# Performance work log

Hardware: AMD Instinct MI355X
Metric: run time of the kernel (lower is better)

The kernel has to match this reference:

```python
import jax, jax.numpy as jnp
import numpy as np

N, E = 50000, 800000
IN_CH, OUT_CH = 128, 16
H1, D1 = 2, 2 * OUT_CH           # conv1: heads=2, per-head dim 32, concat -> 64
MID = H1 * D1                    # 64
NEG_SLOPE = 0.2

def setup_inputs() -> dict:
    key = jax.random.key(0)
    ks = jax.random.split(key, 16)
    s = lambda k, shape: jax.random.normal(k, shape, dtype=jnp.float32) * 0.1
    return {
        "x": jax.random.normal(ks[0], (N, IN_CH), dtype=jnp.float32),
        "edge_index": jax.random.randint(ks[1], (2, E), 0, N, dtype=jnp.int64),
        "W1": s(ks[2], (IN_CH, H1 * D1)),
        "att_src1": s(ks[3], (H1, D1)),
        "att_dst1": s(ks[4], (H1, D1)),
        "b1": jnp.zeros((MID,), jnp.float32),
        "W_mu": s(ks[5], (MID, OUT_CH)),
        "att_src_mu": s(ks[6], (1, OUT_CH)),
        "att_dst_mu": s(ks[7], (1, OUT_CH)),
        "b_mu": jnp.zeros((OUT_CH,), jnp.float32),
        "W_ls": s(ks[8], (MID, OUT_CH)),
        "att_src_ls": s(ks[9], (1, OUT_CH)),
        "att_dst_ls": s(ks[10], (1, OUT_CH)),
        "b_ls": jnp.zeros((OUT_CH,), jnp.float32),
    }

def gat_conv(x, src, dst, W, att_src, att_dst, bias, heads, d):
    # x: [N, F]; src/dst: [E'] (self loops included); PyG GATConv, eval mode (dropout off)
    n = x.shape[0]
    h = (x @ W).reshape(n, heads, d)                     # [N, H, D]
    a_src = jnp.sum(h * att_src, axis=-1)                # [N, H]
    a_dst = jnp.sum(h * att_dst, axis=-1)                # [N, H]
    e = jax.nn.leaky_relu(a_src[src] + a_dst[dst], NEG_SLOPE)   # [E', H]
    # segment softmax over incoming edges of each destination node
    m = jax.ops.segment_max(e, dst, num_segments=n)
    ex = jnp.exp(e - m[dst])
    denom = jax.ops.segment_sum(ex, dst, num_segments=n)
    alpha = ex / (denom[dst] + 1e-16)                    # [E', H]
    msg = h[src] * alpha[:, :, None]                     # [E', H, D]
    out = jax.ops.segment_sum(msg, dst, num_segments=n)  # [N, H, D]
    return out, bias

def reference(x, edge_index, W1, att_src1, att_dst1, b1,
              W_mu, att_src_mu, att_dst_mu, b_mu,
              W_ls, att_src_ls, att_dst_ls, b_ls):
    n = x.shape[0]
    loops = jnp.arange(n, dtype=edge_index.dtype)
    src = jnp.concatenate([edge_index[0], loops])        # add_self_loops=True (inputs have none)
    dst = jnp.concatenate([edge_index[1], loops])
    h, b = gat_conv(x, src, dst, W1, att_src1, att_dst1, b1, H1, D1)
    h = jax.nn.relu(h.reshape(n, H1 * D1) + b)           # concat=True -> [N, 64]
    mu, bm = gat_conv(h, src, dst, W_mu, att_src_mu, att_dst_mu, b_mu, 1, OUT_CH)
    ls, bl = gat_conv(h, src, dst, W_ls, att_src_ls, att_dst_ls, b_ls, 1, OUT_CH)
    mu = mu.mean(axis=1) + bm                            # concat=False, heads=1 -> mean == squeeze
    ls = ls.mean(axis=1) + bl
    return (mu, ls)
```

## Files before the change

### kernel.cpp

```cpp
#include <hip/hip_runtime.h>

#define NEG 0.2f

__device__ __forceinline__ float lrelu(float v) { return v > 0.f ? v : NEG * v; }

__device__ __forceinline__ unsigned short f2bf(float f) {
    unsigned u = __float_as_uint(f);
    unsigned r = (u + 0x7FFF + ((u >> 16) & 1)) >> 16;
    return (unsigned short)r;
}
__device__ __forceinline__ float bf_lo(unsigned v) { return __uint_as_float(v << 16); }
__device__ __forceinline__ float bf_hi(unsigned v) { return __uint_as_float(v & 0xffff0000u); }

__global__ void build_w1ext(const float* __restrict__ W1, const float* __restrict__ asrc,
                            const float* __restrict__ adst, float* __restrict__ Wext) {
    int i = blockIdx.x * blockDim.x + threadIdx.x;
    if (i >= 128 * 68) return;
    int k = i / 68, c = i % 68;
    if (c < 64) { Wext[i] = W1[k * 64 + c]; return; }
    int j = c - 64;
    int hh = j & 1;
    const float* att = (j >= 2) ? adst : asrc;
    float s = 0.f;
    for (int d = 0; d < 32; ++d) s += W1[k * 64 + hh * 32 + d] * att[hh * 32 + d];
    Wext[i] = s;
}

__global__ void build_w2ext(const float* __restrict__ Wmu, const float* __restrict__ Wls,
                            const float* __restrict__ asmu, const float* __restrict__ admu,
                            const float* __restrict__ asls, const float* __restrict__ adls,
                            float* __restrict__ Wext) {
    int i = blockIdx.x * blockDim.x + threadIdx.x;
    if (i >= 64 * 36) return;
    int k = i / 36, c = i % 36;
    if (c < 16) { Wext[i] = Wmu[k * 16 + c]; return; }
    if (c < 32) { Wext[i] = Wls[k * 16 + (c - 16)]; return; }
    int j = c - 32;
    const float* W = (j < 2) ? Wmu : Wls;
    const float* att = (j == 0) ? asmu : (j == 1) ? admu : (j == 2) ? asls : adls;
    float s = 0.f;
    for (int c2 = 0; c2 < 16; ++c2) s += W[k * 16 + c2] * att[c2];
    Wext[i] = s;
}

__global__ __launch_bounds__(256) void gemm1(const float* __restrict__ x,
                                             const float* __restrict__ Wext,
                                             unsigned* __restrict__ h32, float* __restrict__ a1, int n) {
    __shared__ float xs[16][129];
    __shared__ float Ws[128][68];
    int t = threadIdx.x;
    int row0 = blockIdx.x * 16;
    for (int i = t; i < 128 * 68; i += 256) Ws[i / 68][i % 68] = Wext[i];
    for (int i = t; i < 16 * 128; i += 256) {
        int r = i >> 7, k = i & 127;
        int gr = row0 + r;
        xs[r][k] = (gr < n) ? x[gr * 128 + k] : 0.f;
    }
    __syncthreads();
    int r = t >> 4, c = t & 15;
    float acc0 = 0, acc1 = 0, acc2 = 0, acc3 = 0;
    for (int k = 0; k < 128; ++k) {
        float xv = xs[r][k];
        acc0 += xv * Ws[k][c * 4 + 0];
        acc1 += xv * Ws[k][c * 4 + 1];
        acc2 += xv * Ws[k][c * 4 + 2];
        acc3 += xv * Ws[k][c * 4 + 3];
    }
    int gr = row0 + r;
    if (gr < n) {
        unsigned p0 = ((unsigned)f2bf(acc1) << 16) | f2bf(acc0);
        unsigned p1 = ((unsigned)f2bf(acc3) << 16) | f2bf(acc2);
        *(uint2*)&h32[gr * 32 + c * 2] = make_uint2(p0, p1);
    }
    if (t < 64) {
        int r2 = t >> 2, j = t & 3;
        float a = 0.f;
        for (int k = 0; k < 128; ++k) a += xs[r2][k] * Ws[k][64 + j];
        if (row0 + r2 < n) a1[(row0 + r2) * 4 + j] = a;
    }
}

__global__ void count_deg(const int* __restrict__ dstv, int E, int* __restrict__ deg) {
    int i = blockIdx.x * blockDim.x + threadIdx.x;
    if (i < E) atomicAdd(&deg[dstv[i]], 1);
}

__global__ __launch_bounds__(256) void block_sums(const int* __restrict__ deg, int n,
                                                  int* __restrict__ bsums) {
    int i = blockIdx.x * 256 + threadIdx.x;
    int v = (i < n) ? deg[i] : 0;
    for (int o = 32; o > 0; o >>= 1) v += __shfl_down(v, o, 64);
    __shared__ int ws[4];
    if ((threadIdx.x & 63) == 0) ws[threadIdx.x >> 6] = v;
    __syncthreads();
    if (threadIdx.x == 0) bsums[blockIdx.x] = ws[0] + ws[1] + ws[2] + ws[3];
}

__global__ __launch_bounds__(256) void scan_bsums(int* __restrict__ bsums, int nb) {
    __shared__ int s[256];
    int t = threadIdx.x;
    int v = (t < nb) ? bsums[t] : 0;
    s[t] = v;
    __syncthreads();
    for (int o = 1; o < 256; o <<= 1) {
        int u = (t >= o) ? s[t - o] : 0;
        __syncthreads();
        s[t] += u;
        __syncthreads();
    }
    if (t < nb) bsums[t] = s[t] - v;
}

__global__ __launch_bounds__(256) void write_offs(const int* __restrict__ deg,
                                                  const int* __restrict__ bsums, int n,
                                                  int* __restrict__ offs, int* __restrict__ cursor) {
    int t = threadIdx.x;
    int i = blockIdx.x * 256 + t;
    int v = (i < n) ? deg[i] : 0;
    __shared__ int s[256];
    s[t] = v;
    __syncthreads();
    for (int o = 1; o < 256; o <<= 1) {
        int u = (t >= o) ? s[t - o] : 0;
        __syncthreads();
        s[t] += u;
        __syncthreads();
    }
    int excl = s[t] - v + bsums[blockIdx.x];
    if (i < n) { offs[i] = excl; cursor[i] = excl; }
    if (i == n - 1) offs[n] = excl + v;
}

__global__ void scatter_edges(const int* __restrict__ srcv, const int* __restrict__ dstv, int E,
                              int* __restrict__ cursor, int* __restrict__ srcs) {
    int i = blockIdx.x * blockDim.x + threadIdx.x;
    if (i < E) {
        int d = dstv[i];
        int slot = atomicAdd(&cursor[d], 1);
        srcs[slot] = srcv[i];
    }
}

__global__ __launch_bounds__(256) void agg1(const unsigned* __restrict__ h32, const float* __restrict__ a1,
                                            const int* __restrict__ offs, const int* __restrict__ srcs,
                                            const float* __restrict__ b1, float* __restrict__ h1, int n) {
    int wid = threadIdx.x >> 6, lane = threadIdx.x & 63;
    int node = blockIdx.x * 4 + wid;
    if (node >= n) return;
    int half = lane >> 5;
    int l = lane & 31;
    int head = l >> 4;
    float adst = a1[node * 4 + 2 + head];
    float acc0 = 0.f, acc1 = 0.f, denom = 0.f;
    if (half == 0) {
        float w = __expf(lrelu(a1[node * 4 + head] + adst));
        unsigned hv = h32[node * 32 + l];
        acc0 = w * bf_lo(hv); acc1 = w * bf_hi(hv);
        denom = w;
    }
    int kb = offs[node], ke = offs[node + 1];
    for (int k = kb + half; k < ke; k += 2) {
        int s = srcs[k];
        float wv = __expf(lrelu(a1[s * 4 + head] + adst));
        unsigned hv = h32[s * 32 + l];
        denom += wv;
        acc0 += wv * bf_lo(hv);
        acc1 += wv * bf_hi(hv);
    }
    acc0  += __shfl(acc0,  lane ^ 32, 64);
    acc1  += __shfl(acc1,  lane ^ 32, 64);
    denom += __shfl(denom, lane ^ 32, 64);
    if (half == 0) {
        float o0 = acc0 / denom + b1[2 * l];
        float o1 = acc1 / denom + b1[2 * l + 1];
        *(float2*)&h1[node * 64 + 2 * l] = make_float2(fmaxf(o0, 0.f), fmaxf(o1, 0.f));
    }
}

__global__ __launch_bounds__(256) void gemm2(const float* __restrict__ h1,
                                             const float* __restrict__ Wext,
                                             unsigned* __restrict__ hml, float* __restrict__ a2, int n) {
    __shared__ float hs[16][65];
    __shared__ float Ws[64][36];
    int t = threadIdx.x;
    int row0 = blockIdx.x * 16;
    for (int i = t; i < 64 * 36; i += 256) Ws[i / 36][i % 36] = Wext[i];
    for (int i = t; i < 16 * 64; i += 256) {
        int r = i >> 6, k = i & 63;
        int gr = row0 + r;
        hs[r][k] = (gr < n) ? h1[gr * 64 + k] : 0.f;
    }
    __syncthreads();
    int r = t >> 4, c = t & 15;
    float am = 0, al = 0;
    for (int k = 0; k < 64; ++k) {
        float hv = hs[r][k];
        am += hv * Ws[k][c];
        al += hv * Ws[k][16 + c];
    }
    int gr = row0 + r;
    if (gr < n) hml[gr * 16 + c] = ((unsigned)f2bf(al) << 16) | f2bf(am);
    if (t < 64) {
        int r2 = t >> 2, j = t & 3;
        float a = 0.f;
        for (int k = 0; k < 64; ++k) a += hs[r2][k] * Ws[k][32 + j];
        if (row0 + r2 < n) a2[(row0 + r2) * 4 + j] = a;
    }
}

__global__ __launch_bounds__(256) void agg2(const unsigned* __restrict__ hml,
                                            const float* __restrict__ a2, const int* __restrict__ offs,
                                            const int* __restrict__ srcs,
                                            const float* __restrict__ bmu, const float* __restrict__ bls,
                                            float* __restrict__ out, int n) {
    int grp = threadIdx.x >> 5;
    int node = blockIdx.x * 8 + grp;
    if (node >= n) return;
    int lane32 = threadIdx.x & 31;
    int half = lane32 >> 4;
    int c = lane32 & 15;
    float admu = a2[node * 4 + 1], adls = a2[node * 4 + 3];
    float amu = 0.f, als = 0.f, dmu = 0.f, dls = 0.f;
    if (half == 0) {
        float wmu = __expf(lrelu(a2[node * 4 + 0] + admu));
        float wls = __expf(lrelu(a2[node * 4 + 2] + adls));
        unsigned hv = hml[node * 16 + c];
        amu = wmu * bf_lo(hv); als = wls * bf_hi(hv);
        dmu = wmu; dls = wls;
    }
    int kb = offs[node], ke = offs[node + 1];
    for (int k = kb + half; k < ke; k += 2) {
        int s = srcs[k];
        float4 av = *(const float4*)&a2[s * 4];
        float w1v = __expf(lrelu(av.x + admu));
        float w2v = __expf(lrelu(av.z + adls));
        unsigned hv = hml[s * 16 + c];
        dmu += w1v; dls += w2v;
        amu += w1v * bf_lo(hv);
        als += w2v * bf_hi(hv);
    }
    amu += __shfl_xor(amu, 16, 64);
    als += __shfl_xor(als, 16, 64);
    dmu += __shfl_xor(dmu, 16, 64);
    dls += __shfl_xor(dls, 16, 64);
    if (half == 0) {
        out[node * 16 + c] = amu / dmu + bmu[c];
        out[(size_t)n * 16 + node * 16 + c] = als / dls + bls[c];
    }
}

extern "C" void kernel_launch(void* const* d_in, const int* in_sizes, int n_in,
                              void* d_out, int out_size, void* d_ws, size_t ws_size,
                              hipStream_t stream) {
    const float* x    = (const float*)d_in[0];
    const int*   ei   = (const int*)d_in[1];
    const float* W1   = (const float*)d_in[2];
    const float* as1  = (const float*)d_in[3];
    const float* ad1  = (const float*)d_in[4];
    const float* b1   = (const float*)d_in[5];
    const float* Wmu  = (const float*)d_in[6];
    const float* asmu = (const float*)d_in[7];
    const float* admu = (const float*)d_in[8];
    const float* bmu  = (const float*)d_in[9];
    const float* Wls  = (const float*)d_in[10];
    const float* asls = (const float*)d_in[11];
    const float* adls = (const float*)d_in[12];
    const float* bls  = (const float*)d_in[13];
    float* out = (float*)d_out;

    int n = in_sizes[0] / 128;
    int E = in_sizes[1] / 2;

    char* ws = (char*)d_ws;
    size_t off = 0;
    auto alloc = [&](size_t b) { size_t p = off; off = (off + b + 255) & ~(size_t)255; return p; };

    unsigned* h32 = (unsigned*)(ws + alloc((size_t)n * 32 * 4));
    float*    h1  = (float*)(ws + alloc((size_t)n * 64 * 4));
    float*    a1  = (float*)(ws + alloc((size_t)n * 4 * 4));
    unsigned* hml = (unsigned*)(ws + alloc((size_t)n * 16 * 4));
    float*    a2  = (float*)(ws + alloc((size_t)n * 4 * 4));
    float*    w1e = (float*)(ws + alloc(128 * 68 * 4));
    float*    w2e = (float*)(ws + alloc(64 * 36 * 4));
    int*   deg    = (int*)(ws + alloc((size_t)n * 4));
    int*   offs   = (int*)(ws + alloc((size_t)(n + 1) * 4));
    int*   cursor = (int*)(ws + alloc((size_t)n * 4));
    int*   srcs   = (int*)(ws + alloc((size_t)E * 4));
    int*   bsums  = (int*)(ws + alloc(1024 * 4));

    int nb = (n + 255) / 256;

    hipMemsetAsync(deg, 0, (size_t)n * 4, stream);
    build_w1ext<<<(128 * 68 + 255) / 256, 256, 0, stream>>>(W1, as1, ad1, w1e);
    build_w2ext<<<(64 * 36 + 255) / 256, 256, 0, stream>>>(Wmu, Wls, asmu, admu, asls, adls, w2e);
    gemm1<<<(n + 15) / 16, 256, 0, stream>>>(x, w1e, h32, a1, n);
    count_deg<<<(E + 255) / 256, 256, 0, stream>>>(ei + E, E, deg);
    block_sums<<<nb, 256, 0, stream>>>(deg, n, bsums);
    scan_bsums<<<1, 256, 0, stream>>>(bsums, nb);
    write_offs<<<nb, 256, 0, stream>>>(deg, bsums, n, offs, cursor);
    scatter_edges<<<(E + 255) / 256, 256, 0, stream>>>(ei, ei + E, E, cursor, srcs);
    agg1<<<(n + 3) / 4, 256, 0, stream>>>(h32, a1, offs, srcs, b1, h1, n);
    gemm2<<<(n + 15) / 16, 256, 0, stream>>>(h1, w2e, hml, a2, n);
    agg2<<<(n + 7) / 8, 256, 0, stream>>>(hml, a2, offs, srcs, bmu, bls, out, n);
}
```

Before: 334.5 us.

## Register-tile gemm1, partition edge atomics by dst range, widen aggregation edge parallelism

```diff
diff --git a/kernel.cpp b/kernel.cpp
--- a/kernel.cpp
+++ b/kernel.cpp
@@ -15,9 +15,10 @@
 __global__ void build_w1ext(const float* __restrict__ W1, const float* __restrict__ asrc,
                             const float* __restrict__ adst, float* __restrict__ Wext) {
     int i = blockIdx.x * blockDim.x + threadIdx.x;
-    if (i >= 128 * 68) return;
-    int k = i / 68, c = i % 68;
+    if (i >= 128 * 80) return;
+    int k = i / 80, c = i % 80;
     if (c < 64) { Wext[i] = W1[k * 64 + c]; return; }
+    if (c >= 68) { Wext[i] = 0.f; return; }
     int j = c - 64;
     int hh = j & 1;
     const float* att = (j >= 2) ? adst : asrc;
@@ -43,46 +44,83 @@
     Wext[i] = s;
 }
 
-__global__ __launch_bounds__(256) void gemm1(const float* __restrict__ x,
+__global__ __launch_bounds__(320) void gemm1(const float* __restrict__ x,
                                              const float* __restrict__ Wext,
                                              unsigned* __restrict__ h32, float* __restrict__ a1, int n) {
-    __shared__ float xs[16][129];
-    __shared__ float Ws[128][68];
+    __shared__ float xs[64][132];
+    __shared__ float Ws[128][80];
     int t = threadIdx.x;
-    int row0 = blockIdx.x * 16;
-    for (int i = t; i < 128 * 68; i += 256) Ws[i / 68][i % 68] = Wext[i];
-    for (int i = t; i < 16 * 128; i += 256) {
-        int r = i >> 7, k = i & 127;
+    int row0 = blockIdx.x * 64;
+    for (int i = t; i < 128 * 20; i += 320) {
+        int r = i / 20, cq = i % 20;
+        *(float4*)&Ws[r][cq * 4] = *(const float4*)&Wext[r * 80 + cq * 4];
+    }
+    for (int i = t; i < 64 * 32; i += 320) {
+        int r = i >> 5, kq = i & 31;
         int gr = row0 + r;
-        xs[r][k] = (gr < n) ? x[gr * 128 + k] : 0.f;
-    }
-    __syncthreads();
-    int r = t >> 4, c = t & 15;
-    float acc0 = 0, acc1 = 0, acc2 = 0, acc3 = 0;
-    for (int k = 0; k < 128; ++k) {
-        float xv = xs[r][k];
-        acc0 += xv * Ws[k][c * 4 + 0];
-        acc1 += xv * Ws[k][c * 4 + 1];
-        acc2 += xv * Ws[k][c * 4 + 2];
-        acc3 += xv * Ws[k][c * 4 + 3];
-    }
-    int gr = row0 + r;
-    if (gr < n) {
-        unsigned p0 = ((unsigned)f2bf(acc1) << 16) | f2bf(acc0);
-        unsigned p1 = ((unsigned)f2bf(acc3) << 16) | f2bf(acc2);
-        *(uint2*)&h32[gr * 32 + c * 2] = make_uint2(p0, p1);
-    }
-    if (t < 64) {
-        int r2 = t >> 2, j = t & 3;
-        float a = 0.f;
-        for (int k = 0; k < 128; ++k) a += xs[r2][k] * Ws[k][64 + j];
-        if (row0 + r2 < n) a1[(row0 + r2) * 4 + j] = a;
-    }
-}
-
-__global__ void count_deg(const int* __restrict__ dstv, int E, int* __restrict__ deg) {
-    int i = blockIdx.x * blockDim.x + threadIdx.x;
-    if (i < E) atomicAdd(&deg[dstv[i]], 1);
+        float4 v = (gr < n) ? *(const float4*)&x[gr * 128 + kq * 4] : make_float4(0, 0, 0, 0);
+        *(float4*)&xs[r][kq * 4] = v;
+    }
+    __syncthreads();
+    int rg = t / 20, cg = t % 20;
+    int r0 = rg * 4, c0 = cg * 4;
+    float4 acc0 = make_float4(0, 0, 0, 0), acc1 = acc0, acc2 = acc0, acc3 = acc0;
+    for (int k = 0; k < 128; k += 4) {
+        float4 w0 = *(float4*)&Ws[k + 0][c0];
+        float4 w1 = *(float4*)&Ws[k + 1][c0];
+        float4 w2 = *(float4*)&Ws[k + 2][c0];
+        float4 w3 = *(float4*)&Ws[k + 3][c0];
+#pragma unroll
+        for (int j = 0; j < 4; ++j) {
+            float4 xv = *(float4*)&xs[r0 + j][k];
+            float4& a = j == 0 ? acc0 : j == 1 ? acc1 : j == 2 ? acc2 : acc3;
+            a.x += xv.x * w0.x + xv.y * w1.x + xv.z * w2.x + xv.w * w3.x;
+            a.y += xv.x * w0.y + xv.y * w1.y + xv.z * w2.y + xv.w * w3.y;
+            a.z += xv.x * w0.z + xv.y * w1.z + xv.z * w2.z + xv.w * w3.z;
+            a.w += xv.x * w0.w + xv.y * w1.w + xv.z * w2.w + xv.w * w3.w;
+        }
+    }
+#pragma unroll
+    for (int j = 0; j < 4; ++j) {
+        int gr = row0 + r0 + j;
+        if (gr >= n) break;
+        float4 a = j == 0 ? acc0 : j == 1 ? acc1 : j == 2 ? acc2 : acc3;
+        if (cg < 16) {
+            unsigned p0 = ((unsigned)f2bf(a.y) << 16) | f2bf(a.x);
+            unsigned p1 = ((unsigned)f2bf(a.w) << 16) | f2bf(a.z);
+            *(uint2*)&h32[gr * 32 + (c0 >> 1)] = make_uint2(p0, p1);
+        } else if (cg == 16) {
+            *(float4*)&a1[gr * 4] = a;
+        }
+    }
+}
+
+__global__ __launch_bounds__(256) void count_deg_part(const int* __restrict__ dstv, int E, int np,
+                                                      int* __restrict__ deg) {
+    int p = blockIdx.x & 7;
+    int bslot = blockIdx.x >> 3;
+    int nblk = gridDim.x >> 3;
+    int lo = p * np, hi = lo + np;
+    for (int i = bslot * 256 + threadIdx.x; i < E; i += nblk * 256) {
+        int d = dstv[i];
+        if (d >= lo && d < hi) atomicAdd(&deg[d], 1);
+    }
+}
+
+__global__ __launch_bounds__(256) void scatter_part(const int* __restrict__ srcv,
+                                                    const int* __restrict__ dstv, int E, int np,
+                                                    int* __restrict__ cursor, int* __restrict__ srcs) {
+    int p = blockIdx.x & 7;
+    int bslot = blockIdx.x >> 3;
+    int nblk = gridDim.x >> 3;
+    int lo = p * np, hi = lo + np;
+    for (int i = bslot * 256 + threadIdx.x; i < E; i += nblk * 256) {
+        int d = dstv[i];
+        if (d >= lo && d < hi) {
+            int slot = atomicAdd(&cursor[d], 1);
+            srcs[slot] = srcv[i];
+        }
+    }
 }
 
 __global__ __launch_bounds__(256) void block_sums(const int* __restrict__ deg, int n,
@@ -131,49 +169,46 @@
     if (i == n - 1) offs[n] = excl + v;
 }
 
-__global__ void scatter_edges(const int* __restrict__ srcv, const int* __restrict__ dstv, int E,
-                              int* __restrict__ cursor, int* __restrict__ srcs) {
-    int i = blockIdx.x * blockDim.x + threadIdx.x;
-    if (i < E) {
-        int d = dstv[i];
-        int slot = atomicAdd(&cursor[d], 1);
-        srcs[slot] = srcv[i];
-    }
-}
-
 __global__ __launch_bounds__(256) void agg1(const unsigned* __restrict__ h32, const float* __restrict__ a1,
                                             const int* __restrict__ offs, const int* __restrict__ srcs,
                                             const float* __restrict__ b1, float* __restrict__ h1, int n) {
     int wid = threadIdx.x >> 6, lane = threadIdx.x & 63;
     int node = blockIdx.x * 4 + wid;
     if (node >= n) return;
-    int half = lane >> 5;
-    int l = lane & 31;
-    int head = l >> 4;
+    int q = lane >> 4;
+    int l = lane & 15;
+    int head = l >> 3;
     float adst = a1[node * 4 + 2 + head];
-    float acc0 = 0.f, acc1 = 0.f, denom = 0.f;
-    if (half == 0) {
+    float ax = 0.f, ay = 0.f, az = 0.f, aw = 0.f, denom = 0.f;
+    if (q == 0) {
         float w = __expf(lrelu(a1[node * 4 + head] + adst));
-        unsigned hv = h32[node * 32 + l];
-        acc0 = w * bf_lo(hv); acc1 = w * bf_hi(hv);
+        uint2 hv = *(const uint2*)&h32[node * 32 + 2 * l];
+        ax = w * bf_lo(hv.x); ay = w * bf_hi(hv.x);
+        az = w * bf_lo(hv.y); aw = w * bf_hi(hv.y);
         denom = w;
     }
     int kb = offs[node], ke = offs[node + 1];
-    for (int k = kb + half; k < ke; k += 2) {
+    for (int k = kb + q; k < ke; k += 4) {
         int s = srcs[k];
         float wv = __expf(lrelu(a1[s * 4 + head] + adst));
-        unsigned hv = h32[s * 32 + l];
+        uint2 hv = *(const uint2*)&h32[s * 32 + 2 * l];
         denom += wv;
-        acc0 += wv * bf_lo(hv);
-        acc1 += wv * bf_hi(hv);
-    }
-    acc0  += __shfl(acc0,  lane ^ 32, 64);
-    acc1  += __shfl(acc1,  lane ^ 32, 64);
-    denom += __shfl(denom, lane ^ 32, 64);
-    if (half == 0) {
-        float o0 = acc0 / denom + b1[2 * l];
-        float o1 = acc1 / denom + b1[2 * l + 1];
-        *(float2*)&h1[node * 64 + 2 * l] = make_float2(fmaxf(o0, 0.f), fmaxf(o1, 0.f));
+        ax += wv * bf_lo(hv.x); ay += wv * bf_hi(hv.x);
+        az += wv * bf_lo(hv.y); aw += wv * bf_hi(hv.y);
+    }
+    ax += __shfl_xor(ax, 16, 64); ax += __shfl_xor(ax, 32, 64);
+    ay += __shfl_xor(ay, 16, 64); ay += __shfl_xor(ay, 32, 64);
+    az += __shfl_xor(az, 16, 64); az += __shfl_xor(az, 32, 64);
+    aw += __shfl_xor(aw, 16, 64); aw += __shfl_xor(aw, 32, 64);
+    denom += __shfl_xor(denom, 16, 64); denom += __shfl_xor(denom, 32, 64);
+    if (q == 0) {
+        float4 bv = *(const float4*)&b1[4 * l];
+        float4 o;
+        o.x = fmaxf(ax / denom + bv.x, 0.f);
+        o.y = fmaxf(ay / denom + bv.y, 0.f);
+        o.z = fmaxf(az / denom + bv.z, 0.f);
+        o.w = fmaxf(aw / denom + bv.w, 0.f);
+        *(float4*)&h1[node * 64 + 4 * l] = o;
     }
 }
 
@@ -213,15 +248,13 @@
                                             const int* __restrict__ srcs,
                                             const float* __restrict__ bmu, const float* __restrict__ bls,
                                             float* __restrict__ out, int n) {
-    int grp = threadIdx.x >> 5;
-    int node = blockIdx.x * 8 + grp;
+    int wid = threadIdx.x >> 6, lane = threadIdx.x & 63;
+    int node = blockIdx.x * 4 + wid;
     if (node >= n) return;
-    int lane32 = threadIdx.x & 31;
-    int half = lane32 >> 4;
-    int c = lane32 & 15;
+    int q = lane >> 4, c = lane & 15;
     float admu = a2[node * 4 + 1], adls = a2[node * 4 + 3];
     float amu = 0.f, als = 0.f, dmu = 0.f, dls = 0.f;
-    if (half == 0) {
+    if (q == 0) {
         float wmu = __expf(lrelu(a2[node * 4 + 0] + admu));
         float wls = __expf(lrelu(a2[node * 4 + 2] + adls));
         unsigned hv = hml[node * 16 + c];
@@ -229,7 +262,7 @@
         dmu = wmu; dls = wls;
     }
     int kb = offs[node], ke = offs[node + 1];
-    for (int k = kb + half; k < ke; k += 2) {
+    for (int k = kb + q; k < ke; k += 4) {
         int s = srcs[k];
         float4 av = *(const float4*)&a2[s * 4];
         float w1v = __expf(lrelu(av.x + admu));
@@ -239,11 +272,11 @@
         amu += w1v * bf_lo(hv);
         als += w2v * bf_hi(hv);
     }
-    amu += __shfl_xor(amu, 16, 64);
-    als += __shfl_xor(als, 16, 64);
-    dmu += __shfl_xor(dmu, 16, 64);
-    dls += __shfl_xor(dls, 16, 64);
-    if (half == 0) {
+    amu += __shfl_xor(amu, 16, 64); amu += __shfl_xor(amu, 32, 64);
+    als += __shfl_xor(als, 16, 64); als += __shfl_xor(als, 32, 64);
+    dmu += __shfl_xor(dmu, 16, 64); dmu += __shfl_xor(dmu, 32, 64);
+    dls += __shfl_xor(dls, 16, 64); dls += __shfl_xor(dls, 32, 64);
+    if (q == 0) {
         out[node * 16 + c] = amu / dmu + bmu[c];
         out[(size_t)n * 16 + node * 16 + c] = als / dls + bls[c];
     }
@@ -270,6 +303,7 @@
 
     int n = in_sizes[0] / 128;
     int E = in_sizes[1] / 2;
+    int np = (n + 7) / 8;
 
     char* ws = (char*)d_ws;
     size_t off = 0;
@@ -280,7 +314,7 @@
     float*    a1  = (float*)(ws + alloc((size_t)n * 4 * 4));
     unsigned* hml = (unsigned*)(ws + alloc((size_t)n * 16 * 4));
     float*    a2  = (float*)(ws + alloc((size_t)n * 4 * 4));
-    float*    w1e = (float*)(ws + alloc(128 * 68 * 4));
+    float*    w1e = (float*)(ws + alloc(128 * 80 * 4));
     float*    w2e = (float*)(ws + alloc(64 * 36 * 4));
     int*   deg    = (int*)(ws + alloc((size_t)n * 4));
     int*   offs   = (int*)(ws + alloc((size_t)(n + 1) * 4));
@@ -291,15 +325,15 @@
     int nb = (n + 255) / 256;
 
     hipMemsetAsync(deg, 0, (size_t)n * 4, stream);
-    build_w1ext<<<(128 * 68 + 255) / 256, 256, 0, stream>>>(W1, as1, ad1, w1e);
+    build_w1ext<<<(128 * 80 + 255) / 256, 256, 0, stream>>>(W1, as1, ad1, w1e);
     build_w2ext<<<(64 * 36 + 255) / 256, 256, 0, stream>>>(Wmu, Wls, asmu, admu, asls, adls, w2e);
-    gemm1<<<(n + 15) / 16, 256, 0, stream>>>(x, w1e, h32, a1, n);
-    count_deg<<<(E + 255) / 256, 256, 0, stream>>>(ei + E, E, deg);
+    gemm1<<<(n + 63) / 64, 320, 0, stream>>>(x, w1e, h32, a1, n);
+    count_deg_part<<<2048, 256, 0, stream>>>(ei + E, E, np, deg);
     block_sums<<<nb, 256, 0, stream>>>(deg, n, bsums);
     scan_bsums<<<1, 256, 0, stream>>>(bsums, nb);
     write_offs<<<nb, 256, 0, stream>>>(deg, bsums, n, offs, cursor);
-    scatter_edges<<<(E + 255) / 256, 256, 0, stream>>>(ei, ei + E, E, cursor, srcs);
+    scatter_part<<<2048, 256, 0, stream>>>(ei, ei + E, E, np, cursor, srcs);
     agg1<<<(n + 3) / 4, 256, 0, stream>>>(h32, a1, offs, srcs, b1, h1, n);
     gemm2<<<(n + 15) / 16, 256, 0, stream>>>(h1, w2e, hml, a2, n);
-    agg2<<<(n + 7) / 8, 256, 0, stream>>>(hml, a2, offs, srcs, bmu, bls, out, n);
-}
+    agg2<<<(n + 3) / 4, 256, 0, stream>>>(hml, a2, offs, srcs, bmu, bls, out, n);
+}
```

Result: faster. 304.2 us (-9.1%).
